# Kernel tuning notes

Measured on AMD Instinct MI355X. Metric: run time of the kernel, lower is better.

Reference implementation:

```python
import jax, jax.numpy as jnp
import numpy as np

LAMBDA1 = 0.3366
LAMBDA2 = 0.2424
LAMBDA3 = 0.06
LR = 0.1
N_ITERS = 10          # fixed iteration count standing in for the eps-based while loop
BETA1, BETA2, ADAM_EPS = 0.9, 0.999, 1e-8


def setup_inputs() -> dict:
    key = jax.random.key(0)
    k1, k2, k3 = jax.random.split(key, 3)
    D, T, K = 512, 50000, 16
    return {
        "embedding": jax.random.normal(k1, (D, T), jnp.float32),
        "basis_init": jax.random.normal(k2, (D, K), jnp.float32),
        "activation_init": jax.random.normal(k3, (K, T), jnp.float32),
        "k": K,
    }


def _matrix_l1(X):
    # torch.linalg.norm(X, ord=1) on a 2D tensor = induced 1-norm = max column abs-sum
    return jnp.max(jnp.sum(jnp.abs(X), axis=0))


def _jitter(A):
    # temporal jitter penalty: sum of abs frame-to-frame differences
    return jnp.sum(jnp.abs(A[:, 1:] - A[:, :-1]))


def _shrink(X):
    # faithful to the (buggy) torch _shrink: sign(X) * max(0, |X - lr*l|)
    return jnp.sign(X) * jnp.maximum(0.0, jnp.abs(X - LR * LAMBDA1))


def _adam(p, g, m, v, t):
    m = BETA1 * m + (1.0 - BETA1) * g
    v = BETA2 * v + (1.0 - BETA2) * g * g
    mh = m / (1.0 - BETA1 ** t)
    vh = v / (1.0 - BETA2 ** t)
    p = p - LR * mh / (jnp.sqrt(vh) + ADAM_EPS)
    return p, m, v


def _run(embedding, basis_init, activation_init):
    A = activation_init  # optimizer_act.step() is never called in the source -> A is constant

    def loss_from_B(B):
        return (_matrix_l1(embedding - B @ A)
                + LAMBDA1 * _matrix_l1(B)
                + LAMBDA2 * _matrix_l1(A)
                + LAMBDA3 * _jitter(A))

    # iteration 1: loss is computed on the raw parameter (shrink applied after the step)
    P = basis_init
    m = jnp.zeros_like(P)
    v = jnp.zeros_like(P)
    g = jax.grad(loss_from_B)(P)
    P, m, v = _adam(P, g, m, v, jnp.float32(1.0))

    # iterations 2..N: loss sees shrink(P); gradient flows through the shrink into P
    def step(carry, t):
        P, m, v = carry
        g = jax.grad(lambda p: loss_from_B(_shrink(p)))(P)
        P, m, v = _adam(P, g, m, v, t)
        return (P, m, v), None

    ts = jnp.arange(2, N_ITERS + 1, dtype=jnp.float32)
    (P, m, v), _ = jax.lax.scan(step, (P, m, v), ts)
    return _shrink(P), A


def reference(embedding, basis_init, activation_init, k):
    # returns (embedding_basis_matrix, activation_matrix) as in OutputDiarization
    return _run(embedding, basis_init, activation_init)
```

## Files before the change

### kernel.cpp

```cpp
#include <hip/hip_runtime.h>
#include <hip/hip_cooperative_groups.h>

namespace cg = cooperative_groups;

#define D 512
#define T 50000
#define K 16
#define NIT 10

#define NBLK 256
#define BTH  512
#define COLS_PER_BLOCK 196
#define NGRP 49
#define PASSES 2
#define TILE_LD 196
#define TILE_FLOATS (D * TILE_LD)

#define LAMBDA1 0.3366f
#define LR      0.1f
#define SHRINK_C (LR * LAMBDA1)
#define BETA1   0.9f
#define BETA2   0.999f
#define ADAM_EPS 1e-8f

__device__ __forceinline__ float sgn(float x) {
    return (x > 0.f) ? 1.f : ((x < 0.f) ? -1.f : 0.f);
}

__device__ __forceinline__ void accum_row(const float4 e, const float* __restrict__ brow,
                                          const float4* __restrict__ a4, float4& acc) {
    float bb[K];
    *reinterpret_cast<float4*>(&bb[0])  = reinterpret_cast<const float4*>(brow)[0];
    *reinterpret_cast<float4*>(&bb[4])  = reinterpret_cast<const float4*>(brow)[1];
    *reinterpret_cast<float4*>(&bb[8])  = reinterpret_cast<const float4*>(brow)[2];
    *reinterpret_cast<float4*>(&bb[12]) = reinterpret_cast<const float4*>(brow)[3];
    float4 r = e;
#pragma unroll
    for (int k = 0; k < K; ++k) {
        r.x = fmaf(-bb[k], a4[k].x, r.x);
        r.y = fmaf(-bb[k], a4[k].y, r.y);
        r.z = fmaf(-bb[k], a4[k].z, r.z);
        r.w = fmaf(-bb[k], a4[k].w, r.w);
    }
    acc.x += fabsf(r.x); acc.y += fabsf(r.y);
    acc.z += fabsf(r.z); acc.w += fabsf(r.w);
}

__global__ __launch_bounds__(BTH, 2) void diar_all(
        const float* __restrict__ E, const float* __restrict__ Bin,
        const float* __restrict__ A, float* __restrict__ out,
        unsigned long long* __restrict__ slot, float* __restrict__ Et) {
    __shared__ __align__(16) float Bl[D * K];
    __shared__ float4 psum[16][32];
    __shared__ float wsum[8][K];
    __shared__ float colA[K];
    __shared__ int js_s, ks_s;

    const int tid = threadIdx.x;
    const int bid = blockIdx.x;
    cg::grid_group grid = cg::this_grid();

    float pr[K], mr[K], vr[K];
    {
        const float4* src = reinterpret_cast<const float4*>(Bin + tid * K);
        float4* bl4 = reinterpret_cast<float4*>(&Bl[tid * K]);
#pragma unroll
        for (int q = 0; q < 4; ++q) {
            float4 x = src[q];
            bl4[q] = x;
            pr[4 * q + 0] = x.x; pr[4 * q + 1] = x.y;
            pr[4 * q + 2] = x.z; pr[4 * q + 3] = x.w;
        }
#pragma unroll
        for (int k = 0; k < K; ++k) { mr[k] = 0.f; vr[k] = 0.f; }
    }
    if (bid == 0 && tid < NIT) atomicExch(&slot[tid], 0ull);
    __syncthreads();
    grid.sync();

    const int c = tid & 31;
    const int s = tid >> 5;
    float* const tileB = Et + (size_t)bid * TILE_FLOATS;

    float b1p = 1.f, b2p = 1.f;

    for (int it = 1; it <= NIT; ++it) {
        b1p *= BETA1; b2p *= BETA2;

        unsigned long long key = 0ull;
#pragma unroll
        for (int p = 0; p < PASSES; ++p) {
            const int g = p * 32 + c;
            const int j0 = bid * COLS_PER_BLOCK + g * 4;
            const bool ok = (g < NGRP) && (j0 < T);
            float4 acc = {0.f, 0.f, 0.f, 0.f};
            if (ok) {
                float4 a4[K];
#pragma unroll
                for (int k = 0; k < K; ++k)
                    a4[k] = *reinterpret_cast<const float4*>(A + (size_t)k * T + j0);
                const int rbase = s * 32;
                if (it == 1) {
                    const float* Ep = E + j0;
                    float* tw = tileB + g * 4;
#pragma unroll 4
                    for (int ii = 0; ii < 32; ++ii) {
                        const int i = rbase + ii;
                        const float4 e = *reinterpret_cast<const float4*>(Ep + (size_t)i * T);
                        *reinterpret_cast<float4*>(tw + i * TILE_LD) = e;
                        accum_row(e, &Bl[i * K], a4, acc);
                    }
                } else {
                    const float* tr = tileB + g * 4;
#pragma unroll 4
                    for (int ii = 0; ii < 32; ++ii) {
                        const int i = rbase + ii;
                        const float4 e = *reinterpret_cast<const float4*>(tr + i * TILE_LD);
                        accum_row(e, &Bl[i * K], a4, acc);
                    }
                }
            }
            psum[s][c] = acc;
            __syncthreads();
            if (tid < 32) {
                const int gg = p * 32 + tid;
                const int jb = bid * COLS_PER_BLOCK + gg * 4;
                if (gg < NGRP && jb < T) {
                    float4 cs = psum[0][tid];
#pragma unroll
                    for (int q = 1; q < 16; ++q) {
                        float4 pq = psum[q][tid];
                        cs.x += pq.x; cs.y += pq.y; cs.z += pq.z; cs.w += pq.w;
                    }
                    float v4[4] = {cs.x, cs.y, cs.z, cs.w};
#pragma unroll
                    for (int q = 0; q < 4; ++q) {
                        unsigned long long kq =
                            (((unsigned long long)__float_as_uint(v4[q])) << 32)
                            | (unsigned int)(jb + q);
                        if (kq > key) key = kq;
                    }
                }
            }
            __syncthreads();
        }
        if (tid < 64) {
#pragma unroll
            for (int off = 32; off > 0; off >>= 1) {
                unsigned long long o = __shfl_down(key, off, 64);
                if (o > key) key = o;
            }
            if (tid == 0) atomicMax(&slot[it - 1], key);
        }

        grid.sync();

        if (tid == 0) {
            unsigned long long kk = atomicMax(&slot[it - 1], 0ull);
            js_s = (int)(kk & 0xffffffffull);
        }
        __syncthreads();
        const int js = js_s;
        if (tid < K) colA[tid] = A[(size_t)tid * T + js];

        float cb[K];
        {
            const float* brow = &Bl[tid * K];
#pragma unroll
            for (int k = 0; k < K; ++k) cb[k] = fabsf(brow[k]);
#pragma unroll
            for (int off = 32; off > 0; off >>= 1) {
#pragma unroll
                for (int k = 0; k < K; ++k) cb[k] += __shfl_down(cb[k], off, 64);
            }
            if ((tid & 63) == 0) {
                const int w = tid >> 6;
#pragma unroll
                for (int k = 0; k < K; ++k) wsum[w][k] = cb[k];
            }
        }
        __syncthreads();
        if (tid == 0) {
            float best = -1.f; int kb = 0;
#pragma unroll
            for (int k = 0; k < K; ++k) {
                float t = 0.f;
                for (int w = 0; w < 8; ++w) t += wsum[w][k];
                if (t > best) { best = t; kb = k; }
            }
            ks_s = kb;
        }
        __syncthreads();
        const int ks = ks_s;
        const float biasm = 1.f - b1p;
        const float biasv = 1.f - b2p;

        float r = E[(size_t)tid * T + js];
        const float* brow = &Bl[tid * K];
#pragma unroll
        for (int k = 0; k < K; ++k) r = fmaf(-brow[k], colA[k], r);
        const float sg = sgn(r);

#pragma unroll
        for (int k = 0; k < K; ++k) {
            float g = -sg * colA[k];
            if (k == ks) g += LAMBDA1 * sgn(brow[k]);
            float p = pr[k];
            if (it >= 2) g *= sgn(p) * sgn(p - SHRINK_C);
            float mm = BETA1 * mr[k] + (1.f - BETA1) * g;
            float vv = BETA2 * vr[k] + (1.f - BETA2) * g * g;
            mr[k] = mm; vr[k] = vv;
            p -= LR * (mm / biasm) / (sqrtf(vv / biasv) + ADAM_EPS);
            pr[k] = p;
        }
        {
            float4* bl4 = reinterpret_cast<float4*>(&Bl[tid * K]);
#pragma unroll
            for (int q = 0; q < 4; ++q) {
                float4 x;
                x.x = sgn(pr[4 * q + 0]) * fmaxf(0.f, fabsf(pr[4 * q + 0] - SHRINK_C));
                x.y = sgn(pr[4 * q + 1]) * fmaxf(0.f, fabsf(pr[4 * q + 1] - SHRINK_C));
                x.z = sgn(pr[4 * q + 2]) * fmaxf(0.f, fabsf(pr[4 * q + 2] - SHRINK_C));
                x.w = sgn(pr[4 * q + 3]) * fmaxf(0.f, fabsf(pr[4 * q + 3] - SHRINK_C));
                bl4[q] = x;
            }
        }
        __syncthreads();
    }

    if (bid == 0) {
        float4* o4 = reinterpret_cast<float4*>(out);
        const float4* b4 = reinterpret_cast<const float4*>(Bl);
#pragma unroll
        for (int q = 0; q < 4; ++q) o4[tid * 4 + q] = b4[tid * 4 + q];
    }
    {
        float4* o4 = reinterpret_cast<float4*>(out) + (D * K) / 4;
        const float4* a4p = reinterpret_cast<const float4*>(A);
        const int n4 = (K * T) / 4;
        for (int q = bid * BTH + tid; q < n4; q += NBLK * BTH) o4[q] = a4p[q];
    }
}

extern "C" void kernel_launch(void* const* d_in, const int* in_sizes, int n_in,
                              void* d_out, int out_size, void* d_ws, size_t ws_size,
                              hipStream_t stream) {
    const float* E   = (const float*)d_in[0];
    const float* Bin = (const float*)d_in[1];
    const float* A   = (const float*)d_in[2];
    float* out = (float*)d_out;
    unsigned long long* slot = (unsigned long long*)d_ws;
    float* Et = (float*)((char*)d_ws + 1024);

    void* args[] = { (void*)&E, (void*)&Bin, (void*)&A, (void*)&out,
                     (void*)&slot, (void*)&Et };
    hipLaunchCooperativeKernel((void*)diar_all, dim3(NBLK), dim3(BTH),
                               args, 0, stream);
}
```

Before: 906.7 us.

## Replace grid.sync with hierarchical atomic barrier and read embedding directly each iteration

Replaces the per-iteration cooperative grid.sync with a two-level atomic barrier: 16 leaf counters, each padded to its own cache line, feed a root counter that blocks spin on with s_sleep. Drops the per-block workspace copy of the embedding tile, so every iteration re-reads E from global memory in batches of 8 rows to get more loads in flight. The goal is lower barrier latency and simpler memory traffic. The cost is re-reading the 100MB embedding on each of the 10 iterations, and the spin barrier has a guard timeout that could exit early and break correctness.

```diff
diff --git a/kernel.cpp b/kernel.cpp
--- a/kernel.cpp
+++ b/kernel.cpp
@@ -13,8 +13,10 @@
 #define COLS_PER_BLOCK 196
 #define NGRP 49
 #define PASSES 2
-#define TILE_LD 196
-#define TILE_FLOATS (D * TILE_LD)
+
+#define NLEAF 16
+#define BLK_PER_LEAF (NBLK / NLEAF)
+#define BAR_PAD 32
 
 #define LAMBDA1 0.3366f
 #define LR      0.1f
@@ -46,10 +48,28 @@
     acc.z += fabsf(r.z); acc.w += fabsf(r.w);
 }
 
+__device__ __forceinline__ void bar_arrive_wait(unsigned long long* __restrict__ bar,
+                                                int it0, int bid) {
+    unsigned long long* leaf = &bar[(size_t)((it0 * NLEAF) + (bid & (NLEAF - 1))) * BAR_PAD];
+    unsigned long long* root = &bar[(size_t)((NIT * NLEAF) + it0) * BAR_PAD];
+    __threadfence();
+    if (atomicAdd(leaf, 1ull) == (unsigned long long)(BLK_PER_LEAF - 1)) {
+        __threadfence();
+        atomicAdd(root, 1ull);
+    }
+    long long guard = 0;
+    while (__hip_atomic_load(root, __ATOMIC_RELAXED, __HIP_MEMORY_SCOPE_AGENT)
+           < (unsigned long long)NLEAF) {
+        __builtin_amdgcn_s_sleep(2);
+        if (++guard > (1ll << 26)) break;
+    }
+    __threadfence();
+}
+
 __global__ __launch_bounds__(BTH, 2) void diar_all(
         const float* __restrict__ E, const float* __restrict__ Bin,
         const float* __restrict__ A, float* __restrict__ out,
-        unsigned long long* __restrict__ slot, float* __restrict__ Et) {
+        unsigned long long* __restrict__ slot, unsigned long long* __restrict__ bar) {
     __shared__ __align__(16) float Bl[D * K];
     __shared__ float4 psum[16][32];
     __shared__ float wsum[8][K];
@@ -74,13 +94,17 @@
 #pragma unroll
         for (int k = 0; k < K; ++k) { mr[k] = 0.f; vr[k] = 0.f; }
     }
-    if (bid == 0 && tid < NIT) atomicExch(&slot[tid], 0ull);
+    if (bid == 0) {
+        const int nbar = (NIT * NLEAF + NIT) * BAR_PAD;
+        for (int q = tid; q < nbar; q += BTH) bar[q] = 0ull;
+        if (tid < NIT) slot[tid] = 0ull;
+        __threadfence();
+    }
     __syncthreads();
     grid.sync();
 
     const int c = tid & 31;
     const int s = tid >> 5;
-    float* const tileB = Et + (size_t)bid * TILE_FLOATS;
 
     float b1p = 1.f, b2p = 1.f;
 
@@ -100,24 +124,17 @@
                 for (int k = 0; k < K; ++k)
                     a4[k] = *reinterpret_cast<const float4*>(A + (size_t)k * T + j0);
                 const int rbase = s * 32;
-                if (it == 1) {
-                    const float* Ep = E + j0;
-                    float* tw = tileB + g * 4;
-#pragma unroll 4
-                    for (int ii = 0; ii < 32; ++ii) {
-                        const int i = rbase + ii;
-                        const float4 e = *reinterpret_cast<const float4*>(Ep + (size_t)i * T);
-                        *reinterpret_cast<float4*>(tw + i * TILE_LD) = e;
-                        accum_row(e, &Bl[i * K], a4, acc);
-                    }
-                } else {
-                    const float* tr = tileB + g * 4;
-#pragma unroll 4
-                    for (int ii = 0; ii < 32; ++ii) {
-                        const int i = rbase + ii;
-                        const float4 e = *reinterpret_cast<const float4*>(tr + i * TILE_LD);
-                        accum_row(e, &Bl[i * K], a4, acc);
-                    }
+                const float* Ep = E + j0;
+                float4 eb[8];
+#pragma unroll
+                for (int ch = 0; ch < 4; ++ch) {
+#pragma unroll
+                    for (int u = 0; u < 8; ++u)
+                        eb[u] = *reinterpret_cast<const float4*>(
+                            Ep + (size_t)(rbase + ch * 8 + u) * T);
+#pragma unroll
+                    for (int u = 0; u < 8; ++u)
+                        accum_row(eb[u], &Bl[(rbase + ch * 8 + u) * K], a4, acc);
                 }
             }
             psum[s][c] = acc;
@@ -153,9 +170,8 @@
             if (tid == 0) atomicMax(&slot[it - 1], key);
         }
 
-        grid.sync();
-
         if (tid == 0) {
+            bar_arrive_wait(bar, it - 1, bid);
             unsigned long long kk = atomicMax(&slot[it - 1], 0ull);
             js_s = (int)(kk & 0xffffffffull);
         }
@@ -250,10 +266,10 @@
     const float* A   = (const float*)d_in[2];
     float* out = (float*)d_out;
     unsigned long long* slot = (unsigned long long*)d_ws;
-    float* Et = (float*)((char*)d_ws + 1024);
+    unsigned long long* bar  = (unsigned long long*)((char*)d_ws + 1024);
 
     void* args[] = { (void*)&E, (void*)&Bin, (void*)&A, (void*)&out,
-                     (void*)&slot, (void*)&Et };
+                     (void*)&slot, (void*)&bar };
     hipLaunchCooperativeKernel((void*)diar_all, dim3(NBLK), dim3(BTH),
                                args, 0, stream);
 }
```

New measurement: 878.2 us. 3.1% less time.
